# Optimization experiments

Measured on AMD Instinct MI355X. Metric: run time of the kernel, lower is better.

The kernel has to match this reference:

```python
import jax, jax.numpy as jnp
import numpy as np

B, T, H = 1024, 1024, 64


def _lstm_cell(x, h, c, w_ih, w_hh, b_ih, b_hh):
    # gates: [B, 4H] in PyTorch order i, f, g, o
    g = x @ w_ih.T + h @ w_hh.T + b_ih + b_hh
    i, f, gg, o = jnp.split(g, 4, axis=-1)
    i = jax.nn.sigmoid(i)
    f = jax.nn.sigmoid(f)
    gg = jnp.tanh(gg)
    o = jax.nn.sigmoid(o)
    c_new = f * c + i * gg
    h_new = o * jnp.tanh(c_new)
    return h_new, c_new


def setup_inputs() -> dict:
    key = jax.random.key(0)
    ks = jax.random.split(key, 12)
    s = 1.0 / np.sqrt(H)  # torch default init scale
    r = lambda k, shape: jax.random.normal(k, shape, dtype=jnp.float32) * s
    return {
        "x": jax.random.normal(ks[0], (B, T), dtype=jnp.float32),
        "w_ih1": r(ks[1], (4 * H, 1)),
        "w_hh1": r(ks[2], (4 * H, H)),
        "b_ih1": r(ks[3], (4 * H,)),
        "b_hh1": r(ks[4], (4 * H,)),
        "w_ih2": r(ks[5], (4 * H, H)),
        "w_hh2": r(ks[6], (4 * H, H)),
        "b_ih2": r(ks[7], (4 * H,)),
        "b_hh2": r(ks[8], (4 * H,)),
        "w_lin": r(ks[9], (1, H)),
        "b_lin": r(ks[10], (1,)),
        "future_preds": 0,
    }


def reference(x, w_ih1, w_hh1, b_ih1, b_hh1, w_ih2, w_hh2, b_ih2, b_hh2,
              w_lin, b_lin, future_preds):
    bsz = x.shape[0]
    h1 = jnp.zeros((bsz, H), x.dtype)
    c1 = jnp.zeros((bsz, H), x.dtype)
    h2 = jnp.zeros((bsz, H), x.dtype)
    c2 = jnp.zeros((bsz, H), x.dtype)

    def step(carry, x_t):
        h1, c1, h2, c2 = carry
        h1, c1 = _lstm_cell(x_t, h1, c1, w_ih1, w_hh1, b_ih1, b_hh1)
        h2, c2 = _lstm_cell(h1, h2, c2, w_ih2, w_hh2, b_ih2, b_hh2)
        out = h2 @ w_lin.T + b_lin  # [B, 1]
        return (h1, c1, h2, c2), out

    xs = x.T[:, :, None]  # [T, B, 1]
    carry, outs = jax.lax.scan(step, (h1, c1, h2, c2), xs)
    outputs = outs[:, :, 0].T  # [B, T]

    if future_preds > 0:
        last = outs[-1]  # [B, 1]

        def fstep(carry, _):
            h1, c1, h2, c2, prev = carry
            h1, c1 = _lstm_cell(prev, h1, c1, w_ih1, w_hh1, b_ih1, b_hh1)
            h2, c2 = _lstm_cell(h1, h2, c2, w_ih2, w_hh2, b_ih2, b_hh2)
            out = h2 @ w_lin.T + b_lin
            return (h1, c1, h2, c2, out), out

        _, fouts = jax.lax.scan(fstep, (*carry, last), None, length=future_preds)
        outputs = jnp.concatenate([outputs, fouts[:, :, 0].T], axis=1)

    return outputs
```

## Files before the change

kernel.cpp:

```cpp
#include <hip/hip_runtime.h>
#include <hip/hip_bf16.h>


typedef _Float16 f16x8 __attribute__((ext_vector_type(8)));
typedef float    f32x4 __attribute__((ext_vector_type(4)));

namespace {
constexpr int Bb = 1024;
constexpr int Tt = 1024;
constexpr int NBat = 4;
constexpr int HSTR = 80;
constexpr int XSTR = 1025;

__device__ __forceinline__ float sigm_pre(float a) {
    return __builtin_amdgcn_rcpf(1.0f + __builtin_amdgcn_exp2f(a));
}
__device__ __forceinline__ float tanh_pre(float a) {
    return fmaf(2.0f, __builtin_amdgcn_rcpf(1.0f + __builtin_amdgcn_exp2f(a)), -1.0f);
}
__device__ __forceinline__ float tanh_f(float x) {
    float e = __builtin_amdgcn_exp2f(-2.8853900817779268f * x);
    return fmaf(2.0f, __builtin_amdgcn_rcpf(1.0f + e), -1.0f);
}
__device__ __forceinline__ bool detect_f32(const void* w) {
    const unsigned short* p = (const unsigned short*)w;
    int sane = 0;
    for (int i = 0; i < 64; ++i) {
        int e = (p[2 * i] >> 7) & 0xFF;
        if (e >= 107 && e <= 129) ++sane;
    }
    return sane < 32;
}
__device__ __forceinline__ float ld(const void* p, int i, bool f32) {
    return f32 ? ((const float*)p)[i]
               : __bfloat162float(((const __hip_bfloat16*)p)[i]);
}
__device__ __forceinline__ void st(void* p, int i, float v, bool f32) {
    if (f32) ((float*)p)[i] = v;
    else     ((__hip_bfloat16*)p)[i] = __float2bfloat16(v);
}
__device__ __forceinline__ void poll_flags(const int* f, int tp, int tq, int lane) {
    const int idx = lane & 7;
    const int thr = (idx < 4) ? tp : tq;
    for (;;) {
        int v = ((const volatile int*)f)[idx];
        if (__all(v >= thr)) break;
    }
    __builtin_amdgcn_sched_barrier(0);
    asm volatile("" ::: "memory");
}
}

__global__ __launch_bounds__(512, 1) void lstm2_kernel(
    const void* __restrict__ x,
    const void* __restrict__ w_ih1,
    const void* __restrict__ w_hh1,
    const void* __restrict__ b_ih1,
    const void* __restrict__ b_hh1,
    const void* __restrict__ w_ih2,
    const void* __restrict__ w_hh2,
    const void* __restrict__ b_ih2,
    const void* __restrict__ b_hh2,
    const void* __restrict__ w_lin,
    const void* __restrict__ b_lin,
    void* __restrict__ out)
{
    const int tid  = threadIdx.x;
    const int lane = tid & 63;
    const int w    = tid >> 6;
    const int gw   = w & 3;
    const bool isP = w < 4;
    const int m    = lane & 15;
    const int quad = lane >> 4;
    const int bb   = blockIdx.x * NBat;

    const bool f32 = detect_f32(w_hh1);

    __shared__ float                  xs[NBat * XSTR];
    __shared__ __align__(16) _Float16 h1ring[4][NBat * HSTR];
    __shared__ __align__(16) _Float16 h2buf[2][NBat * HSTR];
    __shared__ __align__(16) float    headp[2][NBat][16];
    __shared__ float                  outbuf[NBat * Tt];
    __shared__ int                    flg[8];

    for (int i = tid; i < NBat * 1024; i += 512)
        xs[(i >> 10) * XSTR + (i & 1023)] = ld(x, (bb + (i >> 10)) * Tt + (i & 1023), f32);
    for (int i = tid; i < NBat * HSTR; i += 512) {
        h1ring[0][i] = (_Float16)0; h1ring[1][i] = (_Float16)0;
        h1ring[2][i] = (_Float16)0; h1ring[3][i] = (_Float16)0;
        h2buf[0][i] = (_Float16)0;  h2buf[1][i] = (_Float16)0;
    }
    if (tid < 8) flg[tid] = 0;

    const int arow = lane & 15;
    const int g_ld = arow & 3;
    const int u_ld = arow >> 2;
    const float scA = (g_ld == 2) ? -2.8853900817779268f : -1.4426950408889634f;
    f16x8 wfA[4][2], wfB[4][2];
    {
        const void* MA = isP ? w_hh1 : w_ih2;
#pragma unroll
        for (int q = 0; q < 4; ++q) {
            const int row = 64 * g_ld + 16 * gw + 4 * q + u_ld;
#pragma unroll
            for (int s = 0; s < 2; ++s) {
                const int base = row * 64 + 32 * s + quad * 8;
                if (f32) {
                    const float* A = (const float*)MA;
                    const float* B = (const float*)w_hh2;
#pragma unroll
                    for (int j = 0; j < 8; ++j) {
                        wfA[q][s][j] = (_Float16)(scA * A[base + j]);
                        wfB[q][s][j] = isP ? (_Float16)0.0f
                                           : (_Float16)(scA * B[base + j]);
                    }
                } else {
                    const __hip_bfloat16* A = (const __hip_bfloat16*)MA;
                    const __hip_bfloat16* B = (const __hip_bfloat16*)w_hh2;
#pragma unroll
                    for (int j = 0; j < 8; ++j) {
                        wfA[q][s][j] = (_Float16)(scA * __bfloat162float(A[base + j]));
                        wfB[q][s][j] = isP ? (_Float16)0.0f
                                           : (_Float16)(scA * __bfloat162float(B[base + j]));
                    }
                }
            }
        }
    }
    f32x4 bv[4], wxv[4];
#pragma unroll
    for (int q = 0; q < 4; ++q)
#pragma unroll
        for (int r = 0; r < 4; ++r) {
            const int row = 64 * r + 16 * gw + 4 * q + quad;
            const float sg = (r == 2) ? -2.8853900817779268f : -1.4426950408889634f;
            bv[q][r] = sg * (isP ? (ld(b_ih1, row, f32) + ld(b_hh1, row, f32))
                                 : (ld(b_ih2, row, f32) + ld(b_hh2, row, f32)));
            wxv[q][r] = isP ? sg * ld(w_ih1, row, f32) : 0.0f;
        }
    const int q2   = m >> 2;
    const int bsel = m & 3;
    const int hidx = bsel * HSTR + 16 * gw + 4 * q2 + quad;
    const bool s1 = (q2 & 1) != 0, s2 = (q2 & 2) != 0;
    const float wl_u = ld(w_lin, 16 * gw + 4 * q2 + quad, f32);
    const float blin = ld(b_lin, 0, f32);
    float cst = 0.0f;
    __syncthreads();

    if (isP) {
#pragma unroll 4
        for (int t = 0; t < Tt; ++t) {
            const float xt = xs[bsel * XSTR + t];
            f32x4 ai[4];
#pragma unroll
            for (int q = 0; q < 4; ++q)
#pragma unroll
                for (int r = 0; r < 4; ++r)
                    ai[q][r] = fmaf(xt, wxv[q][r], bv[q][r]);
            poll_flags(flg, t, t - 3, lane);
            f32x4 acc[4];
            if (t > 0) {
                const _Float16* hp = h1ring[(t - 1) & 3] + bsel * HSTR;
                const f16x8 pa0 = *(const f16x8*)(hp + quad * 8);
                const f16x8 pa1 = *(const f16x8*)(hp + 32 + quad * 8);
                __builtin_amdgcn_s_setprio(1);
#pragma unroll
                for (int q = 0; q < 4; ++q) {
                    f32x4 p0 = __builtin_amdgcn_mfma_f32_16x16x32_f16(wfA[q][0], pa0, ai[q], 0, 0, 0);
                    f32x4 p1 = __builtin_amdgcn_mfma_f32_16x16x32_f16(wfA[q][1], pa1, f32x4{0,0,0,0}, 0, 0, 0);
                    acc[q] = p0 + p1;
                }
                __builtin_amdgcn_s_setprio(0);
            } else {
#pragma unroll
                for (int q = 0; q < 4; ++q) acc[q] = ai[q];
            }
            f32x4 g;
#pragma unroll
            for (int r = 0; r < 4; ++r) {
                float lo = s1 ? acc[1][r] : acc[0][r];
                float hi = s1 ? acc[3][r] : acc[2][r];
                g[r] = s2 ? hi : lo;
            }
            float ig = sigm_pre(g[0]), fg = sigm_pre(g[1]);
            float gg = tanh_pre(g[2]), og = sigm_pre(g[3]);
            cst = fmaf(fg, cst, ig * gg);
            h1ring[t & 3][hidx] = (_Float16)(og * tanh_f(cst));
            if (lane == 0) {
                asm volatile("" ::: "memory");
                *(volatile int*)&flg[gw] = t + 1;
            }
        }
    } else {
#pragma unroll 4
        for (int u = 0; u < Tt; ++u) {
            poll_flags(flg, 0, u, lane);
            if (u > 0 && w == 4 && lane < NBat) {
                const float* hp2 = &headp[(u - 1) & 1][lane][0];
                f32x4 v0 = *(const f32x4*)(hp2);
                f32x4 v1 = *(const f32x4*)(hp2 + 4);
                f32x4 v2 = *(const f32x4*)(hp2 + 8);
                f32x4 v3 = *(const f32x4*)(hp2 + 12);
                f32x4 sv = (v0 + v1) + (v2 + v3);
                outbuf[lane * Tt + (u - 1)] = blin + (sv[0] + sv[1]) + (sv[2] + sv[3]);
            }
            const _Float16* h2p = h2buf[(u + 1) & 1] + bsel * HSTR;
            const f16x8 pb0 = *(const f16x8*)(h2p + quad * 8);
            const f16x8 pb1 = *(const f16x8*)(h2p + 32 + quad * 8);
            f32x4 a3[4];
            __builtin_amdgcn_s_setprio(1);
#pragma unroll
            for (int q = 0; q < 4; ++q) {
                f32x4 p2 = __builtin_amdgcn_mfma_f32_16x16x32_f16(wfB[q][0], pb0, bv[q], 0, 0, 0);
                f32x4 p3 = __builtin_amdgcn_mfma_f32_16x16x32_f16(wfB[q][1], pb1, f32x4{0,0,0,0}, 0, 0, 0);
                a3[q] = p2 + p3;
            }
            __builtin_amdgcn_s_setprio(0);
            poll_flags(flg, u + 1, 0, lane);
            const _Float16* h1p = h1ring[u & 3] + bsel * HSTR;
            const f16x8 pa0 = *(const f16x8*)(h1p + quad * 8);
            const f16x8 pa1 = *(const f16x8*)(h1p + 32 + quad * 8);
            f32x4 acc[4];
            __builtin_amdgcn_s_setprio(1);
#pragma unroll
            for (int q = 0; q < 4; ++q) {
                f32x4 p0 = __builtin_amdgcn_mfma_f32_16x16x32_f16(wfA[q][0], pa0, a3[q], 0, 0, 0);
                f32x4 p1 = __builtin_amdgcn_mfma_f32_16x16x32_f16(wfA[q][1], pa1, f32x4{0,0,0,0}, 0, 0, 0);
                acc[q] = p0 + p1;
            }
            __builtin_amdgcn_s_setprio(0);
            f32x4 g;
#pragma unroll
            for (int r = 0; r < 4; ++r) {
                float lo = s1 ? acc[1][r] : acc[0][r];
                float hi = s1 ? acc[3][r] : acc[2][r];
                g[r] = s2 ? hi : lo;
            }
            float ig = sigm_pre(g[0]), fg = sigm_pre(g[1]);
            float gg = tanh_pre(g[2]), og = sigm_pre(g[3]);
            cst = fmaf(fg, cst, ig * gg);
            float h = og * tanh_f(cst);
            h2buf[u & 1][hidx] = (_Float16)h;
            float p = h * wl_u;
            p += __shfl_xor(p, 16);
            p += __shfl_xor(p, 32);
            if (lane < 16)
                headp[u & 1][bsel][gw * 4 + q2] = p;
            if (lane == 0) {
                asm volatile("" ::: "memory");
                *(volatile int*)&flg[4 + gw] = u + 1;
            }
        }
        if (w == 4) {
            poll_flags(flg, 0, Tt, lane);
            if (lane < NBat) {
                const float* hp2 = &headp[(Tt - 1) & 1][lane][0];
                f32x4 v0 = *(const f32x4*)(hp2);
                f32x4 v1 = *(const f32x4*)(hp2 + 4);
                f32x4 v2 = *(const f32x4*)(hp2 + 8);
                f32x4 v3 = *(const f32x4*)(hp2 + 12);
                f32x4 sv = (v0 + v1) + (v2 + v3);
                outbuf[lane * Tt + (Tt - 1)] = blin + (sv[0] + sv[1]) + (sv[2] + sv[3]);
            }
        }
    }
    __syncthreads();
    for (int i = tid; i < NBat * Tt; i += 512)
        st(out, (bb + (i >> 10)) * Tt + (i & 1023), outbuf[i], f32);
}

extern "C" void kernel_launch(void* const* d_in, const int* in_sizes, int n_in,
                              void* d_out, int out_size, void* d_ws, size_t ws_size,
                              hipStream_t stream)
{
    (void)in_sizes; (void)n_in; (void)out_size; (void)d_ws; (void)ws_size;
    lstm2_kernel<<<dim3(Bb / NBat), dim3(512), 0, stream>>>(
        d_in[0], d_in[1], d_in[2], d_in[3], d_in[4], d_in[5],
        d_in[6], d_in[7], d_in[8], d_in[9], d_in[10], d_out);
}
```

Before: 795.0 us.

## Merge layer-2 flag waits and move head reduction after flag publish

The layer-2 warps now wait once for both the layer-1 step-u flag and the peer layer-2 step-u flags, then issue all eight MFMAs for the input and recurrent terms together instead of splitting them around a second poll. The linear-head partial sum is fully reduced with more shuffles after the step flag is published, so it is off the critical path. A 4-deep headp ring lets the output be written two steps late. The cost is losing the overlap of recurrent MFMAs with waiting on layer 1, and the deeper lag adds ring-indexing risk.

```diff
diff --git a/kernel.cpp b/kernel.cpp
--- a/kernel.cpp
+++ b/kernel.cpp
@@ -79,7 +79,7 @@
     __shared__ float                  xs[NBat * XSTR];
     __shared__ __align__(16) _Float16 h1ring[4][NBat * HSTR];
     __shared__ __align__(16) _Float16 h2buf[2][NBat * HSTR];
-    __shared__ __align__(16) float    headp[2][NBat][16];
+    __shared__ __align__(16) float    headp[4][NBat][4];
     __shared__ float                  outbuf[NBat * Tt];
     __shared__ int                    flg[8];
 
@@ -194,39 +194,26 @@
     } else {
 #pragma unroll 4
         for (int u = 0; u < Tt; ++u) {
-            poll_flags(flg, 0, u, lane);
-            if (u > 0 && w == 4 && lane < NBat) {
-                const float* hp2 = &headp[(u - 1) & 1][lane][0];
-                f32x4 v0 = *(const f32x4*)(hp2);
-                f32x4 v1 = *(const f32x4*)(hp2 + 4);
-                f32x4 v2 = *(const f32x4*)(hp2 + 8);
-                f32x4 v3 = *(const f32x4*)(hp2 + 12);
-                f32x4 sv = (v0 + v1) + (v2 + v3);
-                outbuf[lane * Tt + (u - 1)] = blin + (sv[0] + sv[1]) + (sv[2] + sv[3]);
-            }
+            poll_flags(flg, u + 1, u, lane);
+            if (u > 1 && w == 4 && lane < NBat) {
+                f32x4 v = *(const f32x4*)&headp[(u - 2) & 3][lane][0];
+                outbuf[lane * Tt + (u - 2)] = blin + (v[0] + v[1]) + (v[2] + v[3]);
+            }
+            const _Float16* h1p = h1ring[u & 3] + bsel * HSTR;
             const _Float16* h2p = h2buf[(u + 1) & 1] + bsel * HSTR;
+            const f16x8 pa0 = *(const f16x8*)(h1p + quad * 8);
+            const f16x8 pa1 = *(const f16x8*)(h1p + 32 + quad * 8);
             const f16x8 pb0 = *(const f16x8*)(h2p + quad * 8);
             const f16x8 pb1 = *(const f16x8*)(h2p + 32 + quad * 8);
-            f32x4 a3[4];
-            __builtin_amdgcn_s_setprio(1);
-#pragma unroll
-            for (int q = 0; q < 4; ++q) {
-                f32x4 p2 = __builtin_amdgcn_mfma_f32_16x16x32_f16(wfB[q][0], pb0, bv[q], 0, 0, 0);
-                f32x4 p3 = __builtin_amdgcn_mfma_f32_16x16x32_f16(wfB[q][1], pb1, f32x4{0,0,0,0}, 0, 0, 0);
-                a3[q] = p2 + p3;
-            }
-            __builtin_amdgcn_s_setprio(0);
-            poll_flags(flg, u + 1, 0, lane);
-            const _Float16* h1p = h1ring[u & 3] + bsel * HSTR;
-            const f16x8 pa0 = *(const f16x8*)(h1p + quad * 8);
-            const f16x8 pa1 = *(const f16x8*)(h1p + 32 + quad * 8);
             f32x4 acc[4];
             __builtin_amdgcn_s_setprio(1);
 #pragma unroll
             for (int q = 0; q < 4; ++q) {
-                f32x4 p0 = __builtin_amdgcn_mfma_f32_16x16x32_f16(wfA[q][0], pa0, a3[q], 0, 0, 0);
-                f32x4 p1 = __builtin_amdgcn_mfma_f32_16x16x32_f16(wfA[q][1], pa1, f32x4{0,0,0,0}, 0, 0, 0);
-                acc[q] = p0 + p1;
+                f32x4 p2 = __builtin_amdgcn_mfma_f32_16x16x32_f16(wfA[q][0], pa0, bv[q], 0, 0, 0);
+                p2 = __builtin_amdgcn_mfma_f32_16x16x32_f16(wfA[q][1], pa1, p2, 0, 0, 0);
+                f32x4 p3 = __builtin_amdgcn_mfma_f32_16x16x32_f16(wfB[q][0], pb0, f32x4{0,0,0,0}, 0, 0, 0);
+                p3 = __builtin_amdgcn_mfma_f32_16x16x32_f16(wfB[q][1], pb1, p3, 0, 0, 0);
+                acc[q] = p2 + p3;
             }
             __builtin_amdgcn_s_setprio(0);
             f32x4 g;
@@ -241,26 +228,25 @@
             cst = fmaf(fg, cst, ig * gg);
             float h = og * tanh_f(cst);
             h2buf[u & 1][hidx] = (_Float16)h;
-            float p = h * wl_u;
-            p += __shfl_xor(p, 16);
-            p += __shfl_xor(p, 32);
-            if (lane < 16)
-                headp[u & 1][bsel][gw * 4 + q2] = p;
             if (lane == 0) {
                 asm volatile("" ::: "memory");
                 *(volatile int*)&flg[4 + gw] = u + 1;
             }
+            float p = h * wl_u;
+            p += __shfl_xor(p, 4);
+            p += __shfl_xor(p, 8);
+            p += __shfl_xor(p, 16);
+            p += __shfl_xor(p, 32);
+            if (lane < NBat)
+                headp[u & 3][lane][gw] = p;
         }
         if (w == 4) {
             poll_flags(flg, 0, Tt, lane);
             if (lane < NBat) {
-                const float* hp2 = &headp[(Tt - 1) & 1][lane][0];
-                f32x4 v0 = *(const f32x4*)(hp2);
-                f32x4 v1 = *(const f32x4*)(hp2 + 4);
-                f32x4 v2 = *(const f32x4*)(hp2 + 8);
-                f32x4 v3 = *(const f32x4*)(hp2 + 12);
-                f32x4 sv = (v0 + v1) + (v2 + v3);
-                outbuf[lane * Tt + (Tt - 1)] = blin + (sv[0] + sv[1]) + (sv[2] + sv[3]);
+                f32x4 v2 = *(const f32x4*)&headp[(Tt - 2) & 3][lane][0];
+                outbuf[lane * Tt + (Tt - 2)] = blin + (v2[0] + v2[1]) + (v2[2] + v2[3]);
+                f32x4 v1 = *(const f32x4*)&headp[(Tt - 1) & 3][lane][0];
+                outbuf[lane * Tt + (Tt - 1)] = blin + (v1[0] + v1[1]) + (v1[2] + v1[3]);
             }
         }
     }
```

New measurement: 718.0 us. 9.7% less time.
